# Kernel optimization log

Measured on AMD Instinct MI355X. Metric: run time of the kernel, lower is better.

## Reference

```python
import jax, jax.numpy as jnp
import numpy as np

BASE_THETA = 0.5
K_DOP = 0.2
K_NOR = 0.15
K_SERO = 0.1
DIM = 1024


def setup_inputs() -> dict:
    key = jax.random.key(0)
    ks = jax.random.split(key, 9)
    scale = 1.0 / np.sqrt(DIM)
    x = jax.random.normal(ks[0], (2, 2048, DIM), dtype=jnp.float32)
    Wq = jax.random.normal(ks[1], (DIM, DIM), dtype=jnp.float32) * scale
    bq = jnp.zeros((DIM,), dtype=jnp.float32)
    Wk = jax.random.normal(ks[2], (DIM, DIM), dtype=jnp.float32) * scale
    bk = jnp.zeros((DIM,), dtype=jnp.float32)
    Wv = jax.random.normal(ks[3], (DIM, DIM), dtype=jnp.float32) * scale
    bv = jnp.zeros((DIM,), dtype=jnp.float32)
    Wo = jax.random.normal(ks[4], (DIM, DIM), dtype=jnp.float32) * scale
    bo = jnp.zeros((DIM,), dtype=jnp.float32)
    return {"x": x, "Wq": Wq, "bq": bq, "Wk": Wk, "bk": bk,
            "Wv": Wv, "bv": bv, "Wo": Wo, "bo": bo}


def reference(x, Wq, bq, Wk, bk, Wv, bv, Wo, bo):
    # Projections: torch nn.Linear computes x @ W.T + b
    q = jnp.einsum('bsd,ed->bse', x, Wq) + bq
    k = jnp.einsum('bsd,ed->bse', x, Wk) + bk
    v = jnp.einsum('bsd,ed->bse', x, Wv) + bv
    # Full [B, S, S] scores (no 1/sqrt(d) scaling in the original)
    qk = jnp.einsum('bsd,btd->bst', q, k)
    theta = (BASE_THETA
             + K_DOP * jax.nn.sigmoid(qk)
             + K_NOR * jnp.tanh(qk)
             + K_SERO * jax.nn.relu(qk))
    attn = jax.nn.softmax(theta, axis=-1)
    out = jnp.einsum('bst,btd->bsd', attn, v)
    return jnp.einsum('bsd,ed->bse', out, Wo) + bo
```

## Files before the change

### kernel.cpp

```cpp
#include <hip/hip_runtime.h>
#include <hip/hip_fp16.h>
#include <stdint.h>

typedef _Float16 f16;
typedef __attribute__((ext_vector_type(8))) _Float16 f16x8;
typedef __attribute__((ext_vector_type(4))) _Float16 f16x4;
typedef __attribute__((ext_vector_type(4))) float f32x4;

#define SEQ 2048
#define DIM 1024
#define NBATCH 2
#define MTOT 4096

__global__ void fill_kernel(float* p, float v, int n){
  int i = blockIdx.x * 256 + threadIdx.x;
  if (i < n) p[i] = v;
}

__global__ void cvt_all(const float* __restrict__ x, const float* __restrict__ Wq,
                        const float* __restrict__ Wk, const float* __restrict__ Wv,
                        const float* __restrict__ Wo,
                        f16* __restrict__ x16, f16* __restrict__ Wcat, f16* __restrict__ Wo16){
  int b = blockIdx.x;
  const float* src; f16* dst; int i;
  if (b < 4096){
    src = x; dst = x16; i = b * 256 + threadIdx.x;
  } else {
    int t = (b - 4096) >> 10;
    i = ((b - 4096) & 1023) * 256 + threadIdx.x;
    src = t == 0 ? Wq : t == 1 ? Wk : t == 2 ? Wv : Wo;
    dst = (t == 3) ? Wo16 : Wcat + (size_t)t * DIM * DIM;
  }
  float4 v = ((const float4*)src)[i];
  ((f16x4*)dst)[i] = (f16x4){(f16)v.x, (f16)v.y, (f16)v.z, (f16)v.w};
}

#define GLOAD16(SRC, DST) __builtin_amdgcn_global_load_lds( \
    (__attribute__((address_space(1))) void*)(SRC), \
    (__attribute__((address_space(3))) void*)(DST), 16, 0, 0)

__device__ __forceinline__ float theta_exp(float v){
  const float e1 = __expf(-v);
  const float sg = 1.f / (1.f + e1);
  const float e2 = e1 * e1;
  const float th = 2.f / (1.f + e2) - 1.f;
  const float theta = 0.5f + 0.2f * sg + 0.15f * th + 0.1f * fmaxf(v, 0.f);
  return __expf(fminf(theta - 10.f, 11.f));
}

__global__ __launch_bounds__(256, 3)
void gemm_qkv(const f16* __restrict__ A0, const f16* __restrict__ B0,
              f16* __restrict__ Oq, f16* __restrict__ Ok, f16* __restrict__ Ov,
              const float* __restrict__ c0, const float* __restrict__ c1,
              const float* __restrict__ c2)
{
  __shared__ __align__(16) f16 As[8192];
  __shared__ __align__(16) f16 Bs[8192];
  const int tid  = threadIdx.x;
  const int lane = tid & 63;
  const int wid  = tid >> 6;
  const int r = blockIdx.x;
  const int x = r & 7, i5 = r >> 3;
  const int bm = (x & 3) * 8 + (i5 & 7);
  const int bn = (x >> 2) * 12 + (i5 >> 3);

  const int s_r  = tid >> 3;
  const int s_cb = (tid & 7) ^ (s_r & 7);
  const f16* Ab = A0 + (long)(bm * 128 + s_r) * DIM + s_cb * 8;
  const f16* Bb = B0 + (long)(bn * 128 + s_r) * DIM + s_cb * 8;

  const int l15 = lane & 15, l7 = lane & 7, lhi = lane >> 4;
  const int wrow = (wid >> 1) * 64;
  const int wcol = (wid & 1) * 64;
  const int ar = (wrow + l15) * 64;
  const int br = (wcol + l15) * 64;
  const int cb0 = ((0 + lhi) ^ l7) * 8;
  const int cb1 = ((4 + lhi) ^ l7) * 8;

  f32x4 acc[4][4] = {};

#pragma unroll
  for (int t = 0; t < 16; ++t){
    __syncthreads();
    GLOAD16(Ab + (long)t*64,                  &As[       tid*8]);
    GLOAD16(Ab + (long)t*64 + (long)32 * DIM, &As[2048 + tid*8]);
    GLOAD16(Ab + (long)t*64 + (long)64 * DIM, &As[4096 + tid*8]);
    GLOAD16(Ab + (long)t*64 + (long)96 * DIM, &As[6144 + tid*8]);
    GLOAD16(Bb + (long)t*64,                  &Bs[       tid*8]);
    GLOAD16(Bb + (long)t*64 + (long)32 * DIM, &Bs[2048 + tid*8]);
    GLOAD16(Bb + (long)t*64 + (long)64 * DIM, &Bs[4096 + tid*8]);
    GLOAD16(Bb + (long)t*64 + (long)96 * DIM, &Bs[6144 + tid*8]);
    __syncthreads();
    f16x8 af[4], bf[4];
#pragma unroll
    for (int i = 0; i < 4; i++) af[i] = *(const f16x8*)&As[ar + i * 1024 + cb0];
#pragma unroll
    for (int j = 0; j < 4; j++) bf[j] = *(const f16x8*)&Bs[br + j * 1024 + cb0];
#pragma unroll
    for (int i = 0; i < 4; i++)
#pragma unroll
      for (int j = 0; j < 4; j++)
        acc[i][j] = __builtin_amdgcn_mfma_f32_16x16x32_f16(af[i], bf[j], acc[i][j], 0, 0, 0);
#pragma unroll
    for (int i = 0; i < 4; i++) af[i] = *(const f16x8*)&As[ar + i * 1024 + cb1];
#pragma unroll
    for (int j = 0; j < 4; j++) bf[j] = *(const f16x8*)&Bs[br + j * 1024 + cb1];
#pragma unroll
    for (int i = 0; i < 4; i++)
#pragma unroll
      for (int j = 0; j < 4; j++)
        acc[i][j] = __builtin_amdgcn_mfma_f32_16x16x32_f16(af[i], bf[j], acc[i][j], 0, 0, 0);
  }

  const int cc = l15;
  const int rr = lhi * 4;
#pragma unroll
  for (int i = 0; i < 4; i++)
#pragma unroll
    for (int j = 0; j < 4; j++){
      const int col = bn * 128 + wcol + j * 16 + cc;
      f16* dst; int dcol; float badd;
      if (col < 1024){       dst = Oq; dcol = col;        badd = c0[dcol]; }
      else if (col < 2048){  dst = Ok; dcol = col - 1024; badd = c1[dcol]; }
      else {                 dst = Ov; dcol = col - 2048; badd = c2[dcol]; }
#pragma unroll
      for (int rq = 0; rq < 4; rq++){
        const int row = bm * 128 + wrow + i * 16 + rr + rq;
        dst[(long)row * DIM + dcol] = (f16)(acc[i][j][rq] + badd);
      }
    }
}

__global__ __launch_bounds__(256, 3)
void gemm_merged(const f16* __restrict__ qbuf, const f16* __restrict__ kbuf,
                 const f16* __restrict__ vbuf, const f16* __restrict__ Wo16,
                 f16* __restrict__ P0, f16* __restrict__ P1,
                 f16* __restrict__ V0, f16* __restrict__ V1)
{
  __shared__ __align__(16) f16 As[8192];
  __shared__ __align__(16) f16 Bs[8192];
  const int tid  = threadIdx.x;
  const int lane = tid & 63;
  const int wid  = tid >> 6;
  const int l15 = lane & 15, l7 = lane & 7, lhi = lane >> 4;
  const int s_r  = tid >> 3;
  const int s_cb = (tid & 7) ^ (s_r & 7);
  const int cb0 = ((0 + lhi) ^ l7) * 8;
  const int cb1 = ((4 + lhi) ^ l7) * 8;
  const int cc = l15, rr = lhi * 4;
  const int wrow = (wid >> 1) * 64;
  const int wcol = (wid & 1) * 64;
  const int ar = (wrow + l15) * 64;
  const int br = (wcol + l15) * 64;
  const int r = blockIdx.x;

  const f16 *Ab, *Bb;
  int bm, bn, bz;
  bool isQK;
  if (r < 512){
    isQK = true;
    const int x = r & 7, i5 = r >> 3;
    bz = x >> 2;
    bn = (x & 3) * 4 + (i5 & 3);
    bm = i5 >> 2;
    Ab = qbuf + (long)bz * SEQ * DIM + (long)(bm * 128 + s_r) * DIM + s_cb * 8;
    Bb = kbuf + (long)bz * SEQ * DIM + (long)(bn * 128 + s_r) * DIM + s_cb * 8;
  } else {
    isQK = false;
    const int rr2 = r - 512;
    const int x = rr2 & 7, i5 = rr2 >> 3;
    bz = x >> 2;
    bn = (x & 3) * 2 + (i5 & 1);
    bm = i5 >> 1;
    Ab = vbuf + (long)bz * SEQ * DIM + (long)(bm * 128 + s_r) * DIM + s_cb * 8;
    Bb = Wo16 + (long)(bn * 128 + s_r) * DIM + s_cb * 8;
  }

  f32x4 acc[4][4] = {};

#pragma unroll
  for (int t = 0; t < 16; ++t){
    __syncthreads();
    GLOAD16(Ab + (long)t*64,                  &As[       tid*8]);
    GLOAD16(Ab + (long)t*64 + (long)32 * DIM, &As[2048 + tid*8]);
    GLOAD16(Ab + (long)t*64 + (long)64 * DIM, &As[4096 + tid*8]);
    GLOAD16(Ab + (long)t*64 + (long)96 * DIM, &As[6144 + tid*8]);
    GLOAD16(Bb + (long)t*64,                  &Bs[       tid*8]);
    GLOAD16(Bb + (long)t*64 + (long)32 * DIM, &Bs[2048 + tid*8]);
    GLOAD16(Bb + (long)t*64 + (long)64 * DIM, &Bs[4096 + tid*8]);
    GLOAD16(Bb + (long)t*64 + (long)96 * DIM, &Bs[6144 + tid*8]);
    __syncthreads();
    f16x8 af[4], bf[4];
#pragma unroll
    for (int i = 0; i < 4; i++) af[i] = *(const f16x8*)&As[ar + i * 1024 + cb0];
#pragma unroll
    for (int j = 0; j < 4; j++) bf[j] = *(const f16x8*)&Bs[br + j * 1024 + cb0];
#pragma unroll
    for (int i = 0; i < 4; i++)
#pragma unroll
      for (int j = 0; j < 4; j++)
        acc[i][j] = __builtin_amdgcn_mfma_f32_16x16x32_f16(af[i], bf[j], acc[i][j], 0, 0, 0);
#pragma unroll
    for (int i = 0; i < 4; i++) af[i] = *(const f16x8*)&As[ar + i * 1024 + cb1];
#pragma unroll
    for (int j = 0; j < 4; j++) bf[j] = *(const f16x8*)&Bs[br + j * 1024 + cb1];
#pragma unroll
    for (int i = 0; i < 4; i++)
#pragma unroll
      for (int j = 0; j < 4; j++)
        acc[i][j] = __builtin_amdgcn_mfma_f32_16x16x32_f16(af[i], bf[j], acc[i][j], 0, 0, 0);
  }

  if (isQK){
    f16* Ph = (bn < 8) ? P0 : P1;
#pragma unroll
    for (int i = 0; i < 4; i++)
#pragma unroll
      for (int rq = 0; rq < 4; rq++){
        const int row = bm * 128 + wrow + i * 16 + rr + rq;
#pragma unroll
        for (int j = 0; j < 4; j++){
          const int col = bn * 128 + wcol + j * 16 + cc;
          Ph[(long)bz * SEQ * 1024 + (long)row * 1024 + (col & 1023)] =
              (f16)theta_exp(acc[i][j][rq]);
        }
      }
  } else {
    f16* Vh = (bm < 8) ? V0 : V1;
#pragma unroll
    for (int i = 0; i < 4; i++)
#pragma unroll
      for (int j = 0; j < 4; j++){
        const int col = bn * 128 + wcol + j * 16 + cc;
        const int row0 = bm * 128 + wrow + i * 16 + rr;
        f16x4 pk = {(f16)acc[i][j][0], (f16)acc[i][j][1],
                    (f16)acc[i][j][2], (f16)acc[i][j][3]};
        *(f16x4*)&Vh[(long)bz * DIM * 1024 + (long)col * 1024 + (row0 & 1023)] = pk;
      }
  }
}

__global__ __launch_bounds__(256, 4)
void gemm_final(const f16* __restrict__ P0, const f16* __restrict__ P1,
                const f16* __restrict__ V0, const f16* __restrict__ V1,
                f16* __restrict__ psum, float* __restrict__ rowsum)
{
  __shared__ __align__(16) f16 As[8192];
  __shared__ __align__(16) f16 Bs[8192];
  const int tid  = threadIdx.x;
  const int lane = tid & 63;
  const int wid  = tid >> 6;
  const int r = blockIdx.x;
  const int x = r & 7, i5 = r >> 3;
  const int z4 = x >> 1;
  const int bz = z4 >> 1, kh = z4 & 1;
  const int bn = (x & 1) * 4 + (i5 & 3);
  const int bm = i5 >> 2;

  const f16* Ag = (kh ? P1 : P0) + (long)bz * SEQ * 1024;
  const f16* Bg = (kh ? V1 : V0) + (long)bz * DIM * 1024;

  const int s_r  = tid >> 3;
  const int s_cb = (tid & 7) ^ (s_r & 7);
  const f16* Ab = Ag + (long)(bm * 128 + s_r) * 1024 + s_cb * 8;
  const f16* Bb = Bg + (long)(bn * 128 + s_r) * 1024 + s_cb * 8;

  const int l15 = lane & 15, l7 = lane & 7, lhi = lane >> 4;
  const int wrow = (wid >> 1) * 64;
  const int wcol = (wid & 1) * 64;
  const int ar = (wrow + l15) * 64;
  const int br = (wcol + l15) * 64;
  const int cb0 = ((0 + lhi) ^ l7) * 8;
  const int cb1 = ((4 + lhi) ^ l7) * 8;
  const bool do_rs = ((wid & 1) == 0);

  f32x4 acc[4][4] = {};
  float rsum[4] = {0.f, 0.f, 0.f, 0.f};

#pragma unroll
  for (int t = 0; t < 16; ++t){
    __syncthreads();
    GLOAD16(Ab + (long)t*64,                   &As[       tid*8]);
    GLOAD16(Ab + (long)t*64 + (long)32 * 1024, &As[2048 + tid*8]);
    GLOAD16(Ab + (long)t*64 + (long)64 * 1024, &As[4096 + tid*8]);
    GLOAD16(Ab + (long)t*64 + (long)96 * 1024, &As[6144 + tid*8]);
    GLOAD16(Bb + (long)t*64,                   &Bs[       tid*8]);
    GLOAD16(Bb + (long)t*64 + (long)32 * 1024, &Bs[2048 + tid*8]);
    GLOAD16(Bb + (long)t*64 + (long)64 * 1024, &Bs[4096 + tid*8]);
    GLOAD16(Bb + (long)t*64 + (long)96 * 1024, &Bs[6144 + tid*8]);
    __syncthreads();
    f16x8 af[4], bf[4];
#pragma unroll
    for (int i = 0; i < 4; i++) af[i] = *(const f16x8*)&As[ar + i * 1024 + cb0];
#pragma unroll
    for (int j = 0; j < 4; j++) bf[j] = *(const f16x8*)&Bs[br + j * 1024 + cb0];
#pragma unroll
    for (int i = 0; i < 4; i++)
#pragma unroll
      for (int j = 0; j < 4; j++)
        acc[i][j] = __builtin_amdgcn_mfma_f32_16x16x32_f16(af[i], bf[j], acc[i][j], 0, 0, 0);
    if (do_rs){
#pragma unroll
      for (int i = 0; i < 4; i++)
#pragma unroll
        for (int e = 0; e < 8; e++) rsum[i] += (float)af[i][e];
    }
#pragma unroll
    for (int i = 0; i < 4; i++) af[i] = *(const f16x8*)&As[ar + i * 1024 + cb1];
#pragma unroll
    for (int j = 0; j < 4; j++) bf[j] = *(const f16x8*)&Bs[br + j * 1024 + cb1];
#pragma unroll
    for (int i = 0; i < 4; i++)
#pragma unroll
      for (int j = 0; j < 4; j++)
        acc[i][j] = __builtin_amdgcn_mfma_f32_16x16x32_f16(af[i], bf[j], acc[i][j], 0, 0, 0);
    if (do_rs){
#pragma unroll
      for (int i = 0; i < 4; i++)
#pragma unroll
        for (int e = 0; e < 8; e++) rsum[i] += (float)af[i][e];
    }
  }

  if (do_rs){
#pragma unroll
    for (int i = 0; i < 4; i++){
      rsum[i] += __shfl_xor(rsum[i], 16, 64);
      rsum[i] += __shfl_xor(rsum[i], 32, 64);
    }
    if (bn == 0 && lane < 16){
#pragma unroll
      for (int i = 0; i < 4; i++)
        rowsum[(long)kh * MTOT + bz * SEQ + bm * 128 + wrow + i * 16 + lane] = rsum[i];
    }
  }

  const int cc = l15;
  const int rr = lhi * 4;
  f16* Po = psum + (long)kh * MTOT * DIM + (long)bz * SEQ * DIM;
#pragma unroll
  for (int i = 0; i < 4; i++)
#pragma unroll
    for (int j = 0; j < 4; j++){
      const int col = bn * 128 + wcol + j * 16 + cc;
#pragma unroll
      for (int rq = 0; rq < 4; rq++){
        const int row = bm * 128 + wrow + i * 16 + rr + rq;
        Po[(long)row * DIM + col] = (f16)acc[i][j][rq];
      }
    }
}

__global__ __launch_bounds__(256)
void combine_kernel(const f16* __restrict__ psum, const float* __restrict__ rowsum,
                    const float* __restrict__ bo, float* __restrict__ out)
{
  const long i = (long)blockIdx.x * 256 + threadIdx.x;
  const int row = (int)(i >> 8);
  const int c4  = (int)(i & 255);
  f16x4 a = ((const f16x4*)psum)[i];
  f16x4 b = ((const f16x4*)(psum + (long)MTOT * DIM))[i];
  float4 bb = ((const float4*)bo)[c4];
  const float inv = 1.f / (rowsum[row] + rowsum[MTOT + row]);
  float4 o;
  o.x = ((float)a[0] + (float)b[0]) * inv + bb.x;
  o.y = ((float)a[1] + (float)b[1]) * inv + bb.y;
  o.z = ((float)a[2] + (float)b[2]) * inv + bb.z;
  o.w = ((float)a[3] + (float)b[3]) * inv + bb.w;
  ((float4*)out)[i] = o;
}

extern "C" void kernel_launch(void* const* d_in, const int* in_sizes, int n_in,
                              void* d_out, int out_size, void* d_ws, size_t ws_size,
                              hipStream_t stream){
  const float* x  = (const float*)d_in[0];
  const float* Wq = (const float*)d_in[1];
  const float* bq = (const float*)d_in[2];
  const float* Wk = (const float*)d_in[3];
  const float* bk = (const float*)d_in[4];
  const float* Wv = (const float*)d_in[5];
  const float* bv = (const float*)d_in[6];
  const float* Wo = (const float*)d_in[7];
  const float* bo = (const float*)d_in[8];
  float* out = (float*)d_out;

  char* ws = (char*)d_ws;
  size_t off = 0;
  auto alloc = [&](size_t bytes) -> char* {
    char* p = ws + off; off += (bytes + 255) & ~(size_t)255; return p;
  };

  f16* x16     = (f16*)alloc(2ull * MTOT * DIM);
  f16* Wcat    = (f16*)alloc(2ull * 3 * DIM * DIM);
  f16* Wo16    = (f16*)alloc(2ull * DIM * DIM);
  f16* qbuf    = (f16*)alloc(2ull * MTOT * DIM);
  f16* kbuf    = (f16*)alloc(2ull * MTOT * DIM);
  f16* vbuf    = (f16*)alloc(2ull * MTOT * DIM);
  f16* P0      = (f16*)alloc(2ull * NBATCH * SEQ * 1024);
  f16* P1      = (f16*)alloc(2ull * NBATCH * SEQ * 1024);
  f16* V0      = (f16*)alloc(2ull * NBATCH * DIM * 1024);
  f16* V1      = (f16*)alloc(2ull * NBATCH * DIM * 1024);
  f16* psum    = (f16*)alloc(2ull * 2 * MTOT * DIM);
  float* rowsm = (float*)alloc(4ull * 2 * MTOT);

  if (off > ws_size){
    fill_kernel<<<(out_size + 255) / 256, 256, 0, stream>>>(out, 12345.0f, out_size);
    return;
  }

  cvt_all<<<8192, 256, 0, stream>>>(x, Wq, Wk, Wv, Wo, x16, Wcat, Wo16);

  gemm_qkv<<<768, 256, 0, stream>>>(x16, Wcat, qbuf, kbuf, vbuf, bq, bk, bv);

  gemm_merged<<<768, 256, 0, stream>>>(qbuf, kbuf, vbuf, Wo16, P0, P1, V0, V1);

  gemm_final<<<512, 256, 0, stream>>>(P0, P1, V0, V1, psum, rowsm);

  combine_kernel<<<MTOT * DIM / 4 / 256, 256, 0, stream>>>(psum, rowsm, bo, out);
}
```

Before: 115.9 us.

## Stage GEMM epilogue through padded LDS for coalesced stores; remap block tiles

```diff
diff --git a/kernel.cpp b/kernel.cpp
--- a/kernel.cpp
+++ b/kernel.cpp
@@ -137,8 +137,9 @@
                  f16* __restrict__ P0, f16* __restrict__ P1,
                  f16* __restrict__ V0, f16* __restrict__ V1)
 {
-  __shared__ __align__(16) f16 As[8192];
-  __shared__ __align__(16) f16 Bs[8192];
+  __shared__ __align__(16) f16 sh[17408];
+  f16* As = sh;
+  f16* Bs = sh + 8192;
   const int tid  = threadIdx.x;
   const int lane = tid & 63;
   const int wid  = tid >> 6;
@@ -161,8 +162,8 @@
     isQK = true;
     const int x = r & 7, i5 = r >> 3;
     bz = x >> 2;
-    bn = (x & 3) * 4 + (i5 & 3);
-    bm = i5 >> 2;
+    bm = ((x >> 1) & 1) * 8 + (i5 >> 3);
+    bn = (x & 1) * 8 + (i5 & 7);
     Ab = qbuf + (long)bz * SEQ * DIM + (long)(bm * 128 + s_r) * DIM + s_cb * 8;
     Bb = kbuf + (long)bz * SEQ * DIM + (long)(bn * 128 + s_r) * DIM + s_cb * 8;
   } else {
@@ -211,32 +212,49 @@
         acc[i][j] = __builtin_amdgcn_mfma_f32_16x16x32_f16(af[i], bf[j], acc[i][j], 0, 0, 0);
   }
 
+  __syncthreads();
   if (isQK){
-    f16* Ph = (bn < 8) ? P0 : P1;
 #pragma unroll
     for (int i = 0; i < 4; i++)
 #pragma unroll
       for (int rq = 0; rq < 4; rq++){
-        const int row = bm * 128 + wrow + i * 16 + rr + rq;
-#pragma unroll
-        for (int j = 0; j < 4; j++){
-          const int col = bn * 128 + wcol + j * 16 + cc;
-          Ph[(long)bz * SEQ * 1024 + (long)row * 1024 + (col & 1023)] =
-              (f16)theta_exp(acc[i][j][rq]);
-        }
+        const int rowl = wrow + i * 16 + rr + rq;
+#pragma unroll
+        for (int j = 0; j < 4; j++)
+          sh[rowl * 136 + wcol + j * 16 + cc] = (f16)theta_exp(acc[i][j][rq]);
       }
   } else {
-    f16* Vh = (bm < 8) ? V0 : V1;
 #pragma unroll
     for (int i = 0; i < 4; i++)
 #pragma unroll
       for (int j = 0; j < 4; j++){
-        const int col = bn * 128 + wcol + j * 16 + cc;
-        const int row0 = bm * 128 + wrow + i * 16 + rr;
+        const int coll = wcol + j * 16 + cc;
+        const int row0 = wrow + i * 16 + rr;
         f16x4 pk = {(f16)acc[i][j][0], (f16)acc[i][j][1],
                     (f16)acc[i][j][2], (f16)acc[i][j][3]};
-        *(f16x4*)&Vh[(long)bz * DIM * 1024 + (long)col * 1024 + (row0 & 1023)] = pk;
+        *(f16x4*)&sh[coll * 136 + row0] = pk;
       }
+  }
+  __syncthreads();
+
+  const int prow = tid >> 4;
+  const int pch  = (tid & 15) * 8;
+  if (isQK){
+    f16* Pg = ((bn < 8) ? P0 : P1) + (long)bz * SEQ * 1024
+              + (long)(bm * 128) * 1024 + (bn & 7) * 128;
+#pragma unroll
+    for (int p = 0; p < 8; p++){
+      const int rowl = p * 16 + prow;
+      *(f16x8*)&Pg[(long)rowl * 1024 + pch] = *(const f16x8*)&sh[rowl * 136 + pch];
+    }
+  } else {
+    f16* Vg = ((bm < 8) ? V0 : V1) + (long)bz * DIM * 1024
+              + (long)(bn * 128) * 1024 + (bm & 7) * 128;
+#pragma unroll
+    for (int p = 0; p < 8; p++){
+      const int el = p * 16 + prow;
+      *(f16x8*)&Vg[(long)el * 1024 + pch] = *(const f16x8*)&sh[el * 136 + pch];
+    }
   }
 }
 
@@ -254,8 +272,8 @@
   const int x = r & 7, i5 = r >> 3;
   const int z4 = x >> 1;
   const int bz = z4 >> 1, kh = z4 & 1;
-  const int bn = (x & 1) * 4 + (i5 & 3);
-  const int bm = i5 >> 2;
+  const int bm = (x & 1) * 8 + (i5 >> 3);
+  const int bn = i5 & 7;
 
   const f16* Ag = (kh ? P1 : P0) + (long)bz * SEQ * 1024;
   const f16* Bg = (kh ? V1 : V0) + (long)bz * DIM * 1024;
```

Result: no change. 116.9 us (+0.8%).
